# Optimization experiments

Hardware: AMD Instinct MI355X
Metric: run time of the kernel (lower is better)

Reference implementation:

```python
import jax, jax.numpy as jnp
import numpy as np
from jax import lax

B, T, F_, CIN, COUT, NAUX = 32, 1000, 80, 1, 64, 128
KH, KW = 3, 3            # cnn_ker
CPAD = (1, 1)            # floor(k/2)
CSTR = (1, 1)
PK, PSTR = (2, 2), (2, 2)  # max-pool kernel/stride, pad 0


def setup_inputs() -> dict:
    key = jax.random.key(0)
    k1, k2, k3, k4, k5, k6, k7 = jax.random.split(key, 7)
    x = jax.random.normal(k1, (B, T, F_), dtype=jnp.float32)
    x_len = jax.random.randint(k2, (B,), 0, 1000).astype(jnp.int32)
    aux = jax.random.normal(k3, (B, NAUX), dtype=jnp.float32)
    # hypernetwork (filter/bias generator) params
    Wg = jax.random.normal(k4, (CIN * COUT * KH * KW, NAUX), dtype=jnp.float32) * 0.05
    bg = jax.random.normal(k5, (CIN * COUT * KH * KW,), dtype=jnp.float32) * 0.05
    Wb = jax.random.normal(k6, (COUT, NAUX), dtype=jnp.float32) * 0.05
    bb = jax.random.normal(k7, (COUT,), dtype=jnp.float32) * 0.05
    return {"x": x, "x_len": x_len, "aux": aux, "Wg": Wg, "bg": bg, "Wb": Wb, "bb": bb}


def _calclen(L, p, d, k, s):
    return (L + 2 * p - d * (k - 1) - 1) // s + 1


def reference(x, x_len, aux, Wg, bg, Wb, bb):
    # hypernetwork: per-sample conv filters [B, COUT, CIN, KH, KW] and biases [B, COUT]
    filt = (aux @ Wg.T + bg).reshape(B, COUT, CIN, KH, KW)
    bias = aux @ Wb.T + bb
    # per-sample conv as a single grouped conv: groups = B
    xg = x.reshape(1, B * CIN, T, F_)                 # x is [B, T, F] with CIN=1
    fg = filt.reshape(B * COUT, CIN, KH, KW)
    y = lax.conv_general_dilated(
        xg, fg, window_strides=CSTR,
        padding=[(CPAD[0], CPAD[0]), (CPAD[1], CPAD[1])],
        dimension_numbers=("NCHW", "OIHW", "NCHW"),
        feature_group_count=B)
    y = y.reshape(B, COUT, T, F_) + bias[:, :, None, None]
    # activ = relu
    y = jax.nn.relu(y)
    # max pool (2,2), stride (2,2), no pad
    y = lax.reduce_window(y, -jnp.inf, lax.max,
                          (1, 1, PK[0], PK[1]), (1, 1, PSTR[0], PSTR[1]), "VALID")
    # length propagation + time masking
    l1 = _calclen(x_len, CPAD[0], 1, KH, CSTR[0])
    l2 = _calclen(l1, 0, 1, PK[0], PSTR[0])
    t_out = y.shape[2]
    mask = jnp.arange(t_out)[None, :] >= l2[:, None]          # [B, T_out]
    y = jnp.where(mask[:, None, :, None], jnp.float32(0.0), y)
    return y, l2
```

## Files before the change

### kernel.cpp

```cpp
#include <hip/hip_runtime.h>
#include <hip/hip_fp16.h>
#include <stdint.h>

#define B_    32
#define T_    1000
#define F_    80
#define COUT_ 64
#define NAUX_ 128
#define TO_   500
#define FO_   40
#define PSTR_ 12
#define CL_   16

typedef float v4f __attribute__((ext_vector_type(4)));
typedef _Float16 h2v __attribute__((ext_vector_type(2)));

__global__ __launch_bounds__(256) void hyper_kernel(
    const float* __restrict__ aux,
    const float* __restrict__ Wg,
    const float* __restrict__ bg,
    const float* __restrict__ Wb,
    const float* __restrict__ bb,
    const int*   __restrict__ x_len,
    uint32_t* __restrict__ fw,
    float* __restrict__ l2_out)
{
    const int NFT = B_ * 576 * 4;
    const int NBT = B_ * 64 * 4;
    int t = blockIdx.x * blockDim.x + threadIdx.x;

    if (t < NFT) {
        int d = t >> 2, part = t & 3;
        int b = d / 576, idx = d % 576;
        const float* a = aux + b * NAUX_ + part * 32;
        const float* w = Wg + (size_t)idx * NAUX_ + part * 32;
        float s = 0.f;
        #pragma unroll
        for (int n = 0; n < 32; n += 4) {
            float4 av = *(const float4*)(a + n);
            float4 wv = *(const float4*)(w + n);
            s = fmaf(av.x, wv.x, s);
            s = fmaf(av.y, wv.y, s);
            s = fmaf(av.z, wv.z, s);
            s = fmaf(av.w, wv.w, s);
        }
        s += __shfl_xor(s, 1);
        s += __shfl_xor(s, 2);
        if (part == 0) {
            int c = idx / 9, k = idx % 9;
            uint32_t hu = (uint32_t)__half_as_ushort(__float2half_rn(s + bg[idx]));
            fw[(b * COUT_ + c) * PSTR_ + k] = hu | (hu << 16);
        }
    } else if (t < NFT + NBT) {
        int u = t - NFT;
        int d = u >> 2, part = u & 3;
        int b = d >> 6, c = d & 63;
        const float* a = aux + b * NAUX_ + part * 32;
        const float* w = Wb + c * NAUX_ + part * 32;
        float s = 0.f;
        #pragma unroll
        for (int n = 0; n < 32; n += 4) {
            float4 av = *(const float4*)(a + n);
            float4 wv = *(const float4*)(w + n);
            s = fmaf(av.x, wv.x, s);
            s = fmaf(av.y, wv.y, s);
            s = fmaf(av.z, wv.z, s);
            s = fmaf(av.w, wv.w, s);
        }
        s += __shfl_xor(s, 1);
        s += __shfl_xor(s, 2);
        if (part == 0) fw[d * PSTR_ + 9] = __float_as_uint(s + bb[c]);
    } else if (t < NFT + NBT + B_) {
        int b = t - NFT - NBT;
        l2_out[b] = (float)(x_len[b] >> 1);
    }
}

__global__ __launch_bounds__(256) void conv_pool_kernel(
    const float*    __restrict__ x,
    const int*      __restrict__ x_len,
    const uint32_t* __restrict__ fw,
    float* __restrict__ out)
{
    const int bg  = blockIdx.y;
    const int b   = bg >> 2;
    const int bc0 = bg * CL_;

    int t = blockIdx.x * blockDim.x + threadIdx.x;
    if (t >= TO_ * 10) return;
    int f4 = t % 10;
    int to = t / 10;

    float* obase = out + ((size_t)bc0 * TO_ + to) * FO_ + 4 * f4;

    int l2 = x_len[b] >> 1;
    if (to >= l2) {
        v4f z = (v4f){0.f, 0.f, 0.f, 0.f};
        #pragma unroll
        for (int i = 0; i < CL_; ++i)
            __builtin_nontemporal_store(z, (v4f*)(obase + (size_t)i * (TO_ * FO_)));
        return;
    }

    float w[4][10];
    const float* xb = x + (size_t)b * (T_ * F_);
    const int cbase = 8 * f4;
    #pragma unroll
    for (int i = 0; i < 4; ++i) {
        int r = 2 * to - 1 + i;
        if (r < 0 || r >= T_) {
            #pragma unroll
            for (int j = 0; j < 10; ++j) w[i][j] = 0.f;
        } else {
            const float* rp = xb + r * F_ + cbase;
            w[i][0] = (f4 > 0) ? rp[-1] : 0.f;
            float4 m0 = *(const float4*)(rp);
            float4 m1 = *(const float4*)(rp + 4);
            w[i][1] = m0.x; w[i][2] = m0.y; w[i][3] = m0.z; w[i][4] = m0.w;
            w[i][5] = m1.x; w[i][6] = m1.y; w[i][7] = m1.z; w[i][8] = m1.w;
            w[i][9] = (f4 < 9) ? rp[8] : 0.f;
        }
    }

    __half2 wp[3][10];
    #pragma unroll
    for (int ii = 0; ii < 3; ++ii)
        #pragma unroll
        for (int c = 0; c < 10; ++c)
            wp[ii][c] = __halves2half2(__float2half_rn(w[ii][c]),
                                       __float2half_rn(w[ii + 1][c]));

    const uint32_t* p = fw + (size_t)bc0 * PSTR_;
    #pragma unroll 1
    for (int i = 0; i < CL_; ++i) {
        __half2 flt[9];
        #pragma unroll
        for (int k = 0; k < 9; ++k)
            flt[k] = *(const __half2*)(p + k);
        const float bias = __uint_as_float(p[9]);
        p += PSTR_;

        float o[4];
        #pragma unroll
        for (int q = 0; q < 4; ++q) {
            __half2 acc0 = __halves2half2(__ushort_as_half((unsigned short)0),
                                          __ushort_as_half((unsigned short)0));
            __half2 acc1 = acc0;
            #pragma unroll
            for (int ii = 0; ii < 3; ++ii) {
                #pragma unroll
                for (int jj = 0; jj < 3; ++jj) {
                    const __half2 f = flt[ii * 3 + jj];
                    acc0 = __hfma2(f, wp[ii][2 * q + jj],     acc0);
                    acc1 = __hfma2(f, wp[ii][2 * q + 1 + jj], acc1);
                }
            }
            h2v m2 = __builtin_elementwise_max(*(h2v*)&acc0, *(h2v*)&acc1);
            float m = fmaxf((float)m2.x, (float)m2.y);
            o[q] = fmaxf(m + bias, 0.f);
        }
        v4f ov = (v4f){o[0], o[1], o[2], o[3]};
        __builtin_nontemporal_store(ov, (v4f*)(obase + (size_t)i * (TO_ * FO_)));
    }
}

extern "C" void kernel_launch(void* const* d_in, const int* in_sizes, int n_in,
                              void* d_out, int out_size, void* d_ws, size_t ws_size,
                              hipStream_t stream) {
    const float* x     = (const float*)d_in[0];
    const int*   x_len = (const int*)d_in[1];
    const float* aux   = (const float*)d_in[2];
    const float* Wg    = (const float*)d_in[3];
    const float* bg    = (const float*)d_in[4];
    const float* Wb    = (const float*)d_in[5];
    const float* bb    = (const float*)d_in[6];

    float*    out = (float*)d_out;
    uint32_t* fw  = (uint32_t*)d_ws;
    float* l2_out = out + (size_t)B_ * COUT_ * TO_ * FO_;

    {
        int total = B_ * 576 * 4 + B_ * 64 * 4 + B_;
        int blocks = (total + 255) / 256;
        hipLaunchKernelGGL(hyper_kernel, dim3(blocks), dim3(256), 0, stream,
                           aux, Wg, bg, Wb, bb, x_len, fw, l2_out);
    }
    {
        hipLaunchKernelGGL(conv_pool_kernel, dim3(20, 128), dim3(256), 0, stream,
                           x, x_len, fw, out);
    }
}
```

Before: 46.59 us.

## Fuse hypernetwork filter generation into conv-pool kernel via shared memory

Merges the hypernetwork kernel and the conv/relu/pool kernel into a single launch. Each block computes its 16 channels' filters and bias into shared memory, then runs the conv. The block shape changes to 512 threads, of which 500 do conv work. This removes one kernel launch, the inter-kernel dependency and the global round trip for the filters. In exchange, the hypernetwork dot products are recomputed in every block (10 times per slice), and each block now has a serial prologue before its conv work.

```diff
diff --git a/kernel.cpp b/kernel.cpp
--- a/kernel.cpp
+++ b/kernel.cpp
@@ -9,31 +9,37 @@
 #define NAUX_ 128
 #define TO_   500
 #define FO_   40
-#define PSTR_ 12
 #define CL_   16
 
 typedef float v4f __attribute__((ext_vector_type(4)));
 typedef _Float16 h2v __attribute__((ext_vector_type(2)));
 
-__global__ __launch_bounds__(256) void hyper_kernel(
+__global__ __launch_bounds__(512) void fused_kernel(
+    const float* __restrict__ x,
+    const int*   __restrict__ x_len,
     const float* __restrict__ aux,
     const float* __restrict__ Wg,
-    const float* __restrict__ bg,
+    const float* __restrict__ bgv,
     const float* __restrict__ Wb,
     const float* __restrict__ bb,
-    const int*   __restrict__ x_len,
-    uint32_t* __restrict__ fw,
+    float* __restrict__ out,
     float* __restrict__ l2_out)
 {
-    const int NFT = B_ * 576 * 4;
-    const int NBT = B_ * 64 * 4;
-    int t = blockIdx.x * blockDim.x + threadIdx.x;
+    __shared__ uint32_t params[CL_][10];
 
-    if (t < NFT) {
-        int d = t >> 2, part = t & 3;
-        int b = d / 576, idx = d % 576;
+    const int slice = blockIdx.y;
+    const int b     = slice >> 2;
+    const int g     = slice & 3;
+    const int bc0   = slice * CL_;
+    const int tid   = threadIdx.x;
+
+    for (int task = tid; task < 640; task += 512) {
+        int d = task >> 2, part = task & 3;
+        int ch = d / 10, k = d % 10;
+        int c  = g * CL_ + ch;
         const float* a = aux + b * NAUX_ + part * 32;
-        const float* w = Wg + (size_t)idx * NAUX_ + part * 32;
+        const float* w = (k < 9) ? (Wg + (size_t)(c * 9 + k) * NAUX_ + part * 32)
+                                 : (Wb + (size_t)c * NAUX_ + part * 32);
         float s = 0.f;
         #pragma unroll
         for (int n = 0; n < 32; n += 4) {
@@ -47,54 +53,28 @@
         s += __shfl_xor(s, 1);
         s += __shfl_xor(s, 2);
         if (part == 0) {
-            int c = idx / 9, k = idx % 9;
-            uint32_t hu = (uint32_t)__half_as_ushort(__float2half_rn(s + bg[idx]));
-            fw[(b * COUT_ + c) * PSTR_ + k] = hu | (hu << 16);
+            if (k < 9) {
+                uint32_t hu = (uint32_t)__half_as_ushort(__float2half_rn(s + bgv[c * 9 + k]));
+                params[ch][k] = hu | (hu << 16);
+            } else {
+                params[ch][9] = __float_as_uint(s + bb[c]);
+            }
         }
-    } else if (t < NFT + NBT) {
-        int u = t - NFT;
-        int d = u >> 2, part = u & 3;
-        int b = d >> 6, c = d & 63;
-        const float* a = aux + b * NAUX_ + part * 32;
-        const float* w = Wb + c * NAUX_ + part * 32;
-        float s = 0.f;
-        #pragma unroll
-        for (int n = 0; n < 32; n += 4) {
-            float4 av = *(const float4*)(a + n);
-            float4 wv = *(const float4*)(w + n);
-            s = fmaf(av.x, wv.x, s);
-            s = fmaf(av.y, wv.y, s);
-            s = fmaf(av.z, wv.z, s);
-            s = fmaf(av.w, wv.w, s);
-        }
-        s += __shfl_xor(s, 1);
-        s += __shfl_xor(s, 2);
-        if (part == 0) fw[d * PSTR_ + 9] = __float_as_uint(s + bb[c]);
-    } else if (t < NFT + NBT + B_) {
-        int b = t - NFT - NBT;
-        l2_out[b] = (float)(x_len[b] >> 1);
     }
-}
+    __syncthreads();
 
-__global__ __launch_bounds__(256) void conv_pool_kernel(
-    const float*    __restrict__ x,
-    const int*      __restrict__ x_len,
-    const uint32_t* __restrict__ fw,
-    float* __restrict__ out)
-{
-    const int bg  = blockIdx.y;
-    const int b   = bg >> 2;
-    const int bc0 = bg * CL_;
+    const int xl  = x_len[b];
+    const int l2v = xl >> 1;
+    if (blockIdx.x == 0 && g == 0 && tid == 0) l2_out[b] = (float)l2v;
 
-    int t = blockIdx.x * blockDim.x + threadIdx.x;
-    if (t >= TO_ * 10) return;
-    int f4 = t % 10;
-    int to = t / 10;
+    if (tid >= 500) return;
+    const int pos = blockIdx.x * 500 + tid;
+    const int f4  = pos % 10;
+    const int to  = pos / 10;
 
     float* obase = out + ((size_t)bc0 * TO_ + to) * FO_ + 4 * f4;
 
-    int l2 = x_len[b] >> 1;
-    if (to >= l2) {
+    if (to >= l2v) {
         v4f z = (v4f){0.f, 0.f, 0.f, 0.f};
         #pragma unroll
         for (int i = 0; i < CL_; ++i)
@@ -130,15 +110,13 @@
             wp[ii][c] = __halves2half2(__float2half_rn(w[ii][c]),
                                        __float2half_rn(w[ii + 1][c]));
 
-    const uint32_t* p = fw + (size_t)bc0 * PSTR_;
     #pragma unroll 1
     for (int i = 0; i < CL_; ++i) {
         __half2 flt[9];
         #pragma unroll
         for (int k = 0; k < 9; ++k)
-            flt[k] = *(const __half2*)(p + k);
-        const float bias = __uint_as_float(p[9]);
-        p += PSTR_;
+            flt[k] = *(const __half2*)&params[i][k];
+        const float bias = __uint_as_float(params[i][9]);
 
         float o[4];
         #pragma unroll
@@ -171,22 +149,13 @@
     const int*   x_len = (const int*)d_in[1];
     const float* aux   = (const float*)d_in[2];
     const float* Wg    = (const float*)d_in[3];
-    const float* bg    = (const float*)d_in[4];
+    const float* bgv   = (const float*)d_in[4];
     const float* Wb    = (const float*)d_in[5];
     const float* bb    = (const float*)d_in[6];
 
-    float*    out = (float*)d_out;
-    uint32_t* fw  = (uint32_t*)d_ws;
+    float* out    = (float*)d_out;
     float* l2_out = out + (size_t)B_ * COUT_ * TO_ * FO_;
 
-    {
-        int total = B_ * 576 * 4 + B_ * 64 * 4 + B_;
-        int blocks = (total + 255) / 256;
-        hipLaunchKernelGGL(hyper_kernel, dim3(blocks), dim3(256), 0, stream,
-                           aux, Wg, bg, Wb, bb, x_len, fw, l2_out);
-    }
-    {
-        hipLaunchKernelGGL(conv_pool_kernel, dim3(20, 128), dim3(256), 0, stream,
-                           x, x_len, fw, out);
-    }
+    hipLaunchKernelGGL(fused_kernel, dim3(10, 128), dim3(512), 0, stream,
+                       x, x_len, aux, Wg, bgv, Wb, bb, out, l2_out);
 }
```

New measurement: 57.59 us. +23.6%, slower.

## Split conv channels finer, preload filters to registers, widen hypernet reduction

Applied to the files above, without the earlier changes.

The hypernetwork dot products are spread over 16 lanes instead of 4, which shortens each thread's serial FMA chain and launches more threads. The conv kernel now covers 8 output channels per block instead of 16, doubling the grid. It loads all filter and bias parameters into registers before the fully unrolled channel loop, and packs input pairs to half precision with a round-toward-zero intrinsic. The cost is more redundant input-window loads across blocks and higher register pressure. The rounding mode of the input conversion also changes from round-to-nearest to round-toward-zero.

```diff
diff --git a/kernel.cpp b/kernel.cpp
--- a/kernel.cpp
+++ b/kernel.cpp
@@ -10,10 +10,11 @@
 #define TO_   500
 #define FO_   40
 #define PSTR_ 12
-#define CL_   16
+#define CL_   8
 
 typedef float v4f __attribute__((ext_vector_type(4)));
 typedef _Float16 h2v __attribute__((ext_vector_type(2)));
+typedef __fp16 fp16x2 __attribute__((ext_vector_type(2)));
 
 __global__ __launch_bounds__(256) void hyper_kernel(
     const float* __restrict__ aux,
@@ -25,27 +26,31 @@
     uint32_t* __restrict__ fw,
     float* __restrict__ l2_out)
 {
-    const int NFT = B_ * 576 * 4;
-    const int NBT = B_ * 64 * 4;
+    const int NFT = B_ * 576 * 16;
+    const int NBT = B_ * 64 * 16;
     int t = blockIdx.x * blockDim.x + threadIdx.x;
 
     if (t < NFT) {
-        int d = t >> 2, part = t & 3;
+        int d = t >> 4, part = t & 15;
         int b = d / 576, idx = d % 576;
-        const float* a = aux + b * NAUX_ + part * 32;
-        const float* w = Wg + (size_t)idx * NAUX_ + part * 32;
-        float s = 0.f;
-        #pragma unroll
-        for (int n = 0; n < 32; n += 4) {
-            float4 av = *(const float4*)(a + n);
-            float4 wv = *(const float4*)(w + n);
-            s = fmaf(av.x, wv.x, s);
-            s = fmaf(av.y, wv.y, s);
-            s = fmaf(av.z, wv.z, s);
-            s = fmaf(av.w, wv.w, s);
-        }
+        const float* a = aux + b * NAUX_ + part * 8;
+        const float* w = Wg + (size_t)idx * NAUX_ + part * 8;
+        float4 a0 = *(const float4*)(a);
+        float4 a1 = *(const float4*)(a + 4);
+        float4 w0 = *(const float4*)(w);
+        float4 w1 = *(const float4*)(w + 4);
+        float s = a0.x * w0.x;
+        s = fmaf(a0.y, w0.y, s);
+        s = fmaf(a0.z, w0.z, s);
+        s = fmaf(a0.w, w0.w, s);
+        s = fmaf(a1.x, w1.x, s);
+        s = fmaf(a1.y, w1.y, s);
+        s = fmaf(a1.z, w1.z, s);
+        s = fmaf(a1.w, w1.w, s);
         s += __shfl_xor(s, 1);
         s += __shfl_xor(s, 2);
+        s += __shfl_xor(s, 4);
+        s += __shfl_xor(s, 8);
         if (part == 0) {
             int c = idx / 9, k = idx % 9;
             uint32_t hu = (uint32_t)__half_as_ushort(__float2half_rn(s + bg[idx]));
@@ -53,22 +58,26 @@
         }
     } else if (t < NFT + NBT) {
         int u = t - NFT;
-        int d = u >> 2, part = u & 3;
+        int d = u >> 4, part = u & 15;
         int b = d >> 6, c = d & 63;
-        const float* a = aux + b * NAUX_ + part * 32;
-        const float* w = Wb + c * NAUX_ + part * 32;
-        float s = 0.f;
-        #pragma unroll
-        for (int n = 0; n < 32; n += 4) {
-            float4 av = *(const float4*)(a + n);
-            float4 wv = *(const float4*)(w + n);
-            s = fmaf(av.x, wv.x, s);
-            s = fmaf(av.y, wv.y, s);
-            s = fmaf(av.z, wv.z, s);
-            s = fmaf(av.w, wv.w, s);
-        }
+        const float* a = aux + b * NAUX_ + part * 8;
+        const float* w = Wb + (size_t)c * NAUX_ + part * 8;
+        float4 a0 = *(const float4*)(a);
+        float4 a1 = *(const float4*)(a + 4);
+        float4 w0 = *(const float4*)(w);
+        float4 w1 = *(const float4*)(w + 4);
+        float s = a0.x * w0.x;
+        s = fmaf(a0.y, w0.y, s);
+        s = fmaf(a0.z, w0.z, s);
+        s = fmaf(a0.w, w0.w, s);
+        s = fmaf(a1.x, w1.x, s);
+        s = fmaf(a1.y, w1.y, s);
+        s = fmaf(a1.z, w1.z, s);
+        s = fmaf(a1.w, w1.w, s);
         s += __shfl_xor(s, 1);
         s += __shfl_xor(s, 2);
+        s += __shfl_xor(s, 4);
+        s += __shfl_xor(s, 8);
         if (part == 0) fw[d * PSTR_ + 9] = __float_as_uint(s + bb[c]);
     } else if (t < NFT + NBT + B_) {
         int b = t - NFT - NBT;
@@ -83,7 +92,7 @@
     float* __restrict__ out)
 {
     const int bg  = blockIdx.y;
-    const int b   = bg >> 2;
+    const int b   = bg >> 3;
     const int bc0 = bg * CL_;
 
     int t = blockIdx.x * blockDim.x + threadIdx.x;
@@ -101,6 +110,14 @@
             __builtin_nontemporal_store(z, (v4f*)(obase + (size_t)i * (TO_ * FO_)));
         return;
     }
+
+    const uint32_t* p = fw + (size_t)bc0 * PSTR_;
+    uint32_t prm[CL_][10];
+    #pragma unroll
+    for (int i = 0; i < CL_; ++i)
+        #pragma unroll
+        for (int k = 0; k < 10; ++k)
+            prm[i][k] = p[i * PSTR_ + k];
 
     float w[4][10];
     const float* xb = x + (size_t)b * (T_ * F_);
@@ -126,19 +143,18 @@
     #pragma unroll
     for (int ii = 0; ii < 3; ++ii)
         #pragma unroll
-        for (int c = 0; c < 10; ++c)
-            wp[ii][c] = __halves2half2(__float2half_rn(w[ii][c]),
-                                       __float2half_rn(w[ii + 1][c]));
-
-    const uint32_t* p = fw + (size_t)bc0 * PSTR_;
-    #pragma unroll 1
+        for (int c = 0; c < 10; ++c) {
+            fp16x2 pk = __builtin_amdgcn_cvt_pkrtz(w[ii][c], w[ii + 1][c]);
+            wp[ii][c] = *(__half2*)&pk;
+        }
+
+    #pragma unroll
     for (int i = 0; i < CL_; ++i) {
         __half2 flt[9];
         #pragma unroll
         for (int k = 0; k < 9; ++k)
-            flt[k] = *(const __half2*)(p + k);
-        const float bias = __uint_as_float(p[9]);
-        p += PSTR_;
+            flt[k] = *(const __half2*)&prm[i][k];
+        const float bias = __uint_as_float(prm[i][9]);
 
         float o[4];
         #pragma unroll
@@ -180,13 +196,13 @@
     float* l2_out = out + (size_t)B_ * COUT_ * TO_ * FO_;
 
     {
-        int total = B_ * 576 * 4 + B_ * 64 * 4 + B_;
+        int total = B_ * 576 * 16 + B_ * 64 * 16 + B_;
         int blocks = (total + 255) / 256;
         hipLaunchKernelGGL(hyper_kernel, dim3(blocks), dim3(256), 0, stream,
                            aux, Wg, bg, Wb, bb, x_len, fw, l2_out);
     }
     {
-        hipLaunchKernelGGL(conv_pool_kernel, dim3(20, 128), dim3(256), 0, stream,
+        hipLaunchKernelGGL(conv_pool_kernel, dim3(20, 256), dim3(256), 0, stream,
                            x, x_len, fw, out);
     }
 }
```

New measurement: 43.63 us. -6.3%, faster.
